# Performance work log

Hardware: AMD Instinct MI355X
Metric: run time of the kernel (lower is better)

Reference implementation:

```python
import jax, jax.numpy as jnp
import numpy as np

B, CH, XL, YL = 512, 1, 64, 64
H = 64                       # num_heads
D = CH * XL * YL             # 4096
F = D // H                   # feature_dim = 64 (== H, required by the mask multiply)


def setup_inputs() -> dict:
    key = jax.random.key(0)
    k1, k2, k3, k4, k5 = jax.random.split(key, 5)
    scale = 1.0 / np.sqrt(D)  # roughly kaiming-ish init for square linears
    return {
        "x": jax.random.normal(k1, (B, CH, XL, YL), dtype=jnp.float32),
        "interface_map": jax.random.uniform(k2, (B, CH, XL, YL), dtype=jnp.float32),
        "Wq": jax.random.normal(k3, (D, D), dtype=jnp.float32) * scale,
        "Wk": jax.random.normal(k4, (D, D), dtype=jnp.float32) * scale,
        "Wv": jax.random.normal(k5, (D, D), dtype=jnp.float32) * scale,
    }


def reference(x, interface_map, Wq, Wk, Wv):
    b = x.shape[0]
    xf = x.reshape(b, D)
    # nn.Linear(bias=False): y = x @ W.T
    q = (xf @ Wq.T).reshape(b, H, F)
    k = (xf @ Wk.T).reshape(b, H, F)
    v = (xf @ Wv.T).reshape(b, H, F)
    inv_sqrt_f = jnp.float32(1.0 / np.sqrt(F))
    qk_t = jnp.einsum("bhf,bgf->bhg", q, k) * inv_sqrt_f           # (B, H, H)
    qk_t = qk_t * interface_map.reshape(b, H, F)                   # multiplicative mask (F == H)
    attention_weights = jax.nn.softmax(qk_t, axis=-1)
    weighted_values = jnp.einsum("bhg,bgf->bhf", attention_weights, v)  # (B, H, F)
    combined = jnp.swapaxes(weighted_values, 1, 2).reshape(b, CH, XL, YL)
    output = x * combined
    return output, attention_weights
```

## Files before the change

### kernel.cpp

```cpp
#include <hip/hip_runtime.h>
#include <cstdint>
#include <cstddef>

typedef __attribute__((ext_vector_type(8))) short short8;
typedef __attribute__((ext_vector_type(4))) float f32x4;

#define NB 512
#define DD 4096

__device__ __forceinline__ unsigned short f2bf(float f) {
    unsigned u = __float_as_uint(f);
    u += 0x7fffu + ((u >> 16) & 1u);
    return (unsigned short)(u >> 16);
}
__device__ __forceinline__ unsigned pack2bf(float a, float b) {
    return (unsigned)f2bf(a) | ((unsigned)f2bf(b) << 16);
}

__device__ __forceinline__ void gload_lds16(const void* g, void* l) {
    __builtin_amdgcn_global_load_lds((const __attribute__((address_space(1))) void*)g,
                                     (__attribute__((address_space(3))) void*)l, 16, 0, 0);
}

__global__ __launch_bounds__(256) void cvt_bf16_kernel(const float* __restrict__ src,
                                                       unsigned short* __restrict__ dst,
                                                       int n8) {
    int i = blockIdx.x * 256 + threadIdx.x;
    if (i >= n8) return;
    const float4* s = (const float4*)src + (size_t)i * 2;
    float4 a = s[0], b = s[1];
    uint4 r;
    r.x = pack2bf(a.x, a.y);
    r.y = pack2bf(a.z, a.w);
    r.z = pack2bf(b.x, b.y);
    r.w = pack2bf(b.z, b.w);
    ((uint4*)dst)[i] = r;
}

__global__ __launch_bounds__(256, 2) void gemm_qkv_kernel(
    const unsigned short* __restrict__ xb,
    const float* __restrict__ w0, const float* __restrict__ w1, const float* __restrict__ w2,
    float* __restrict__ qkv)
{
    const int nt = blockIdx.x;
    const int mt = blockIdx.y;
    const int mz = blockIdx.z;
    const float* W = (mz == 0) ? w0 : ((mz == 1) ? w1 : w2);
    float* C = qkv + (size_t)mz * ((size_t)NB * DD);

    __shared__ unsigned short As[2][128 * 64];
    __shared__ unsigned short Bs[2][128 * 64];

    const int t = threadIdx.x;
    const int l = t & 63;
    const int wv = t >> 6;
    const int wr = wv >> 1, wc = wv & 1;

    const unsigned short* Abase = xb + (size_t)(mt * 128) * DD;
    const float* Wbase = W + (size_t)(nt * 128) * DD;

    f32x4 acc[4][4];
    #pragma unroll
    for (int i = 0; i < 4; ++i)
        #pragma unroll
        for (int j = 0; j < 4; ++j)
            acc[i][j] = (f32x4){0.f, 0.f, 0.f, 0.f};

    float4 breg[8];

    #pragma unroll
    for (int p = 0; p < 8; ++p) {
        int qq = p * 256 + t;
        int row = qq >> 4, c4 = qq & 15;
        breg[p] = *(const float4*)(Wbase + (size_t)row * DD + c4 * 4);
    }
    #pragma unroll
    for (int i = 0; i < 4; ++i) {
        int e = i * 256 + t;
        int r = e >> 3;
        int c = ((e & 7) * 8) ^ ((r & 7) * 8);
        gload_lds16(Abase + (size_t)r * DD + c,
                    (char*)(&As[0][0]) + i * 4096 + wv * 1024);
    }
    #pragma unroll
    for (int p = 0; p < 8; ++p) {
        int qq = p * 256 + t;
        int row = qq >> 4, c4 = qq & 15;
        unsigned short* dst = &Bs[0][row * 64 + ((c4 * 4) ^ ((row & 7) * 8))];
        uint2 pk;
        pk.x = pack2bf(breg[p].x, breg[p].y);
        pk.y = pack2bf(breg[p].z, breg[p].w);
        *(uint2*)dst = pk;
    }
    __syncthreads();

    for (int kt = 0; kt < 64; ++kt) {
        const int cur = kt & 1, nxt = cur ^ 1;
        const int kn = (kt + 1) * 64;
        if (kt < 63) {
            #pragma unroll
            for (int p = 0; p < 8; ++p) {
                int qq = p * 256 + t;
                int row = qq >> 4, c4 = qq & 15;
                breg[p] = *(const float4*)(Wbase + (size_t)row * DD + kn + c4 * 4);
            }
            #pragma unroll
            for (int i = 0; i < 4; ++i) {
                int e = i * 256 + t;
                int r = e >> 3;
                int c = ((e & 7) * 8) ^ ((r & 7) * 8);
                gload_lds16(Abase + (size_t)r * DD + kn + c,
                            (char*)(&As[nxt][0]) + i * 4096 + wv * 1024);
            }
        }
        #pragma unroll
        for (int ks = 0; ks < 2; ++ks) {
            short8 af[4], bf[4];
            #pragma unroll
            for (int fi = 0; fi < 4; ++fi) {
                int row = wr * 64 + fi * 16 + (l & 15);
                int off = row * 64 + ((ks * 32 + (l >> 4) * 8) ^ ((row & 7) * 8));
                af[fi] = *(const short8*)(&As[cur][off]);
            }
            #pragma unroll
            for (int fj = 0; fj < 4; ++fj) {
                int row = wc * 64 + fj * 16 + (l & 15);
                int off = row * 64 + ((ks * 32 + (l >> 4) * 8) ^ ((row & 7) * 8));
                bf[fj] = *(const short8*)(&Bs[cur][off]);
            }
            #pragma unroll
            for (int fi = 0; fi < 4; ++fi)
                #pragma unroll
                for (int fj = 0; fj < 4; ++fj)
                    acc[fi][fj] = __builtin_amdgcn_mfma_f32_16x16x32_bf16(af[fi], bf[fj], acc[fi][fj], 0, 0, 0);
        }
        if (kt < 63) {
            #pragma unroll
            for (int p = 0; p < 8; ++p) {
                int qq = p * 256 + t;
                int row = qq >> 4, c4 = qq & 15;
                unsigned short* dst = &Bs[nxt][row * 64 + ((c4 * 4) ^ ((row & 7) * 8))];
                uint2 pk;
                pk.x = pack2bf(breg[p].x, breg[p].y);
                pk.y = pack2bf(breg[p].z, breg[p].w);
                *(uint2*)dst = pk;
            }
        }
        __syncthreads();
    }

    #pragma unroll
    for (int fi = 0; fi < 4; ++fi) {
        int rbase = mt * 128 + wr * 64 + fi * 16 + (l >> 4) * 4;
        #pragma unroll
        for (int fj = 0; fj < 4; ++fj) {
            int col = nt * 128 + wc * 64 + fj * 16 + (l & 15);
            #pragma unroll
            for (int r = 0; r < 4; ++r)
                C[(size_t)(rbase + r) * DD + col] = acc[fi][fj][r];
        }
    }
}

__global__ __launch_bounds__(256) void attn_kernel(
    const float* __restrict__ qkv,
    const float* __restrict__ x,
    const float* __restrict__ imap,
    float* __restrict__ dout)
{
    const int b = blockIdx.x;
    const int t = threadIdx.x;
    const int l = t & 63;
    const int wv = t >> 6;

    __shared__ float sq[64 * 68];
    __shared__ float sk[64 * 68];
    __shared__ float sv[64 * 68];

    const float* qb = qkv + (size_t)b * DD;
    const float* kb = qkv + (size_t)NB * DD + (size_t)b * DD;
    const float* vb = qkv + 2 * (size_t)NB * DD + (size_t)b * DD;

    #pragma unroll
    for (int i = 0; i < 4; ++i) {
        int f4 = i * 256 + t;
        int r = f4 >> 4, c = (f4 & 15) * 4;
        *(float4*)(&sq[r * 68 + c]) = *(const float4*)(qb + (size_t)f4 * 4);
        *(float4*)(&sk[r * 68 + c]) = *(const float4*)(kb + (size_t)f4 * 4);
        *(float4*)(&sv[r * 68 + c]) = *(const float4*)(vb + (size_t)f4 * 4);
    }
    __syncthreads();

    float accs[16];
    #pragma unroll
    for (int i = 0; i < 16; ++i) accs[i] = 0.f;
    #pragma unroll 4
    for (int f4 = 0; f4 < 16; ++f4) {
        float4 kvv = *(const float4*)(&sk[l * 68 + f4 * 4]);
        #pragma unroll
        for (int i = 0; i < 16; ++i) {
            int h = i * 4 + wv;
            float4 qv = *(const float4*)(&sq[h * 68 + f4 * 4]);
            accs[i] = fmaf(qv.x, kvv.x, fmaf(qv.y, kvv.y, fmaf(qv.z, kvv.z, fmaf(qv.w, kvv.w, accs[i]))));
        }
    }
    __syncthreads();
    #pragma unroll
    for (int i = 0; i < 16; ++i) {
        int h = i * 4 + wv;
        float m = imap[(size_t)b * DD + h * 64 + l];
        sk[h * 65 + l] = accs[i] * 0.125f * m;
    }
    __syncthreads();

    {
        int h = t >> 2, j = t & 3;
        float e[16];
        float mx = -3.0e38f;
        #pragma unroll
        for (int q2 = 0; q2 < 16; ++q2) {
            e[q2] = sk[h * 65 + j * 16 + q2];
            mx = fmaxf(mx, e[q2]);
        }
        mx = fmaxf(mx, __shfl_xor(mx, 1));
        mx = fmaxf(mx, __shfl_xor(mx, 2));
        float s = 0.f;
        #pragma unroll
        for (int q2 = 0; q2 < 16; ++q2) { e[q2] = __expf(e[q2] - mx); s += e[q2]; }
        s += __shfl_xor(s, 1);
        s += __shfl_xor(s, 2);
        float invs = 1.0f / s;
        float* aw = dout + (size_t)NB * DD + (size_t)b * DD + h * 64 + j * 16;
        #pragma unroll
        for (int q2 = 0; q2 < 16; q2 += 4) {
            float4 w4 = {e[q2] * invs, e[q2 + 1] * invs, e[q2 + 2] * invs, e[q2 + 3] * invs};
            *(float4*)(aw + q2) = w4;
            sk[h * 65 + j * 16 + q2 + 0] = w4.x;
            sk[h * 65 + j * 16 + q2 + 1] = w4.y;
            sk[h * 65 + j * 16 + q2 + 2] = w4.z;
            sk[h * 65 + j * 16 + q2 + 3] = w4.w;
        }
    }
    __syncthreads();

    float pacc[16];
    #pragma unroll
    for (int i = 0; i < 16; ++i) pacc[i] = 0.f;
    #pragma unroll 4
    for (int g = 0; g < 64; ++g) {
        float p = sk[l * 65 + g];
        const float4* vr = (const float4*)(&sv[g * 68 + wv * 16]);
        float4 v0 = vr[0], v1 = vr[1], v2 = vr[2], v3 = vr[3];
        pacc[0]  = fmaf(p, v0.x, pacc[0]);
        pacc[1]  = fmaf(p, v0.y, pacc[1]);
        pacc[2]  = fmaf(p, v0.z, pacc[2]);
        pacc[3]  = fmaf(p, v0.w, pacc[3]);
        pacc[4]  = fmaf(p, v1.x, pacc[4]);
        pacc[5]  = fmaf(p, v1.y, pacc[5]);
        pacc[6]  = fmaf(p, v1.z, pacc[6]);
        pacc[7]  = fmaf(p, v1.w, pacc[7]);
        pacc[8]  = fmaf(p, v2.x, pacc[8]);
        pacc[9]  = fmaf(p, v2.y, pacc[9]);
        pacc[10] = fmaf(p, v2.z, pacc[10]);
        pacc[11] = fmaf(p, v2.w, pacc[11]);
        pacc[12] = fmaf(p, v3.x, pacc[12]);
        pacc[13] = fmaf(p, v3.y, pacc[13]);
        pacc[14] = fmaf(p, v3.z, pacc[14]);
        pacc[15] = fmaf(p, v3.w, pacc[15]);
    }
    const size_t ob = (size_t)b * DD + (size_t)(wv * 16) * 64 + l;
    #pragma unroll
    for (int ii = 0; ii < 16; ++ii) {
        size_t o = ob + (size_t)ii * 64;
        dout[o] = x[o] * pacc[ii];
    }
}

extern "C" void kernel_launch(void* const* d_in, const int* in_sizes, int n_in,
                              void* d_out, int out_size, void* d_ws, size_t ws_size,
                              hipStream_t stream) {
    const float* x  = (const float*)d_in[0];
    const float* im = (const float*)d_in[1];
    const float* Wq = (const float*)d_in[2];
    const float* Wk = (const float*)d_in[3];
    const float* Wv = (const float*)d_in[4];
    float* out = (float*)d_out;

    unsigned short* xb = (unsigned short*)d_ws;
    float* qkv = (float*)((char*)d_ws + (size_t)NB * DD * 2);

    cvt_bf16_kernel<<<dim3((NB * DD / 8 + 255) / 256), dim3(256), 0, stream>>>(x, xb, NB * DD / 8);

    dim3 gg(32, 4, 3);
    gemm_qkv_kernel<<<gg, dim3(256), 0, stream>>>(xb, Wq, Wk, Wv, qkv);

    attn_kernel<<<dim3(NB), dim3(256), 0, stream>>>(qkv, x, im, out);
}
```

Baseline: 135.3 us.

## Split-K the QKV GEMM with interleaved output layout and smaller K tiles

The QKV projection GEMM now splits the K dimension in two when the workspace is large enough. That doubles the block count (96x4x2 = 768 blocks) to fill more CUs, and the attention kernel sums the two fp32 partials while loading Q/K/V. The K tile shrinks from 64 to 32, the weight-tile LDS buffer becomes single-buffered, and occupancy is raised to 3 blocks per CU. Q/K/V are stored interleaved per row (stride 12288). The cost is extra partial-sum write and read traffic and an additional barrier per K iteration.

```diff
diff --git a/kernel.cpp b/kernel.cpp
--- a/kernel.cpp
+++ b/kernel.cpp
@@ -7,6 +7,7 @@
 
 #define NB 512
 #define DD 4096
+#define NP 12288
 
 __device__ __forceinline__ unsigned short f2bf(float f) {
     unsigned u = __float_as_uint(f);
@@ -37,28 +38,33 @@
     ((uint4*)dst)[i] = r;
 }
 
-__global__ __launch_bounds__(256, 2) void gemm_qkv_kernel(
+template<int KS>
+__global__ __launch_bounds__(256, 3) void gemm_qkv_kernel(
     const unsigned short* __restrict__ xb,
     const float* __restrict__ w0, const float* __restrict__ w1, const float* __restrict__ w2,
-    float* __restrict__ qkv)
+    float* __restrict__ part)
 {
+    constexpr int KLEN = DD / KS;
+    constexpr int NIT = KLEN / 32;
+
     const int nt = blockIdx.x;
     const int mt = blockIdx.y;
-    const int mz = blockIdx.z;
-    const float* W = (mz == 0) ? w0 : ((mz == 1) ? w1 : w2);
-    float* C = qkv + (size_t)mz * ((size_t)NB * DD);
-
-    __shared__ unsigned short As[2][128 * 64];
-    __shared__ unsigned short Bs[2][128 * 64];
+    const int kz = blockIdx.z;
+
+    const float* W = (nt < 32) ? w0 : ((nt < 64) ? w1 : w2);
+    const int ntl = nt & 31;
+    const float* Wbase = W + (size_t)(ntl * 128) * DD + kz * KLEN;
+    const unsigned short* Abase = xb + (size_t)(mt * 128) * DD + kz * KLEN;
+    float* C = part + (size_t)kz * NB * NP;
+
+    __shared__ unsigned short As[2][128 * 32];
+    __shared__ unsigned short Bs[128 * 32];
 
     const int t = threadIdx.x;
     const int l = t & 63;
     const int wv = t >> 6;
     const int wr = wv >> 1, wc = wv & 1;
 
-    const unsigned short* Abase = xb + (size_t)(mt * 128) * DD;
-    const float* Wbase = W + (size_t)(nt * 128) * DD;
-
     f32x4 acc[4][4];
     #pragma unroll
     for (int i = 0; i < 4; ++i)
@@ -66,85 +72,60 @@
         for (int j = 0; j < 4; ++j)
             acc[i][j] = (f32x4){0.f, 0.f, 0.f, 0.f};
 
-    float4 breg[8];
-
-    #pragma unroll
-    for (int p = 0; p < 8; ++p) {
-        int qq = p * 256 + t;
-        int row = qq >> 4, c4 = qq & 15;
-        breg[p] = *(const float4*)(Wbase + (size_t)row * DD + c4 * 4);
-    }
-    #pragma unroll
-    for (int i = 0; i < 4; ++i) {
-        int e = i * 256 + t;
-        int r = e >> 3;
-        int c = ((e & 7) * 8) ^ ((r & 7) * 8);
-        gload_lds16(Abase + (size_t)r * DD + c,
-                    (char*)(&As[0][0]) + i * 4096 + wv * 1024);
-    }
-    #pragma unroll
-    for (int p = 0; p < 8; ++p) {
-        int qq = p * 256 + t;
-        int row = qq >> 4, c4 = qq & 15;
-        unsigned short* dst = &Bs[0][row * 64 + ((c4 * 4) ^ ((row & 7) * 8))];
-        uint2 pk;
-        pk.x = pack2bf(breg[p].x, breg[p].y);
-        pk.y = pack2bf(breg[p].z, breg[p].w);
-        *(uint2*)dst = pk;
-    }
-    __syncthreads();
-
-    for (int kt = 0; kt < 64; ++kt) {
-        const int cur = kt & 1, nxt = cur ^ 1;
-        const int kn = (kt + 1) * 64;
-        if (kt < 63) {
+    const int arow0 = (t >> 2);
+    const int acol  = (((t & 3) ^ ((t >> 3) & 3)) * 8);
+    const int brow = t >> 1, bh = t & 1;
+    const float* wrow = Wbase + (size_t)brow * DD + bh * 16;
+    const int bws = (t >> 2) & 3;
+    char* bw0 = (char*)(&Bs[0]) + brow * 64 + (((2 * bh) ^ bws) * 16);
+    char* bw1 = (char*)(&Bs[0]) + brow * 64 + (((2 * bh + 1) ^ bws) * 16);
+    const int cx = ((l >> 4) ^ ((l >> 1) & 3));
+
+    float4 breg[4];
+
+    #define LOADB(kt)  { _Pragma("unroll") for (int j = 0; j < 4; ++j) \
+                           breg[j] = *(const float4*)(wrow + (kt) * 32 + j * 4); }
+    #define STAGEA(kt, buf) { _Pragma("unroll") for (int i = 0; i < 2; ++i) \
+                           gload_lds16(Abase + (size_t)(i * 64 + arow0) * DD + (kt) * 32 + acol, \
+                                       (char*)(&As[buf][0]) + i * 4096 + wv * 1024); }
+    #define WRITEB()   { uint4 p0, p1; \
+                         p0.x = pack2bf(breg[0].x, breg[0].y); p0.y = pack2bf(breg[0].z, breg[0].w); \
+                         p0.z = pack2bf(breg[1].x, breg[1].y); p0.w = pack2bf(breg[1].z, breg[1].w); \
+                         p1.x = pack2bf(breg[2].x, breg[2].y); p1.y = pack2bf(breg[2].z, breg[2].w); \
+                         p1.z = pack2bf(breg[3].x, breg[3].y); p1.w = pack2bf(breg[3].z, breg[3].w); \
+                         *(uint4*)bw0 = p0; *(uint4*)bw1 = p1; }
+
+    LOADB(0);
+    STAGEA(0, 0);
+    WRITEB();
+    __syncthreads();
+
+    for (int kt = 0; kt < NIT; ++kt) {
+        const int cur = kt & 1;
+        if (kt + 1 < NIT) {
+            STAGEA(kt + 1, cur ^ 1);
+            LOADB(kt + 1);
+        }
+        short8 af[4], bfr[4];
+        #pragma unroll
+        for (int fi = 0; fi < 4; ++fi) {
+            int row = wr * 64 + fi * 16 + (l & 15);
+            af[fi] = *(const short8*)((const char*)(&As[cur][0]) + row * 64 + cx * 16);
+        }
+        #pragma unroll
+        for (int fj = 0; fj < 4; ++fj) {
+            int row = wc * 64 + fj * 16 + (l & 15);
+            bfr[fj] = *(const short8*)((const char*)(&Bs[0]) + row * 64 + cx * 16);
+        }
+        #pragma unroll
+        for (int fi = 0; fi < 4; ++fi)
             #pragma unroll
-            for (int p = 0; p < 8; ++p) {
-                int qq = p * 256 + t;
-                int row = qq >> 4, c4 = qq & 15;
-                breg[p] = *(const float4*)(Wbase + (size_t)row * DD + kn + c4 * 4);
-            }
-            #pragma unroll
-            for (int i = 0; i < 4; ++i) {
-                int e = i * 256 + t;
-                int r = e >> 3;
-                int c = ((e & 7) * 8) ^ ((r & 7) * 8);
-                gload_lds16(Abase + (size_t)r * DD + kn + c,
-                            (char*)(&As[nxt][0]) + i * 4096 + wv * 1024);
-            }
-        }
-        #pragma unroll
-        for (int ks = 0; ks < 2; ++ks) {
-            short8 af[4], bf[4];
-            #pragma unroll
-            for (int fi = 0; fi < 4; ++fi) {
-                int row = wr * 64 + fi * 16 + (l & 15);
-                int off = row * 64 + ((ks * 32 + (l >> 4) * 8) ^ ((row & 7) * 8));
-                af[fi] = *(const short8*)(&As[cur][off]);
-            }
-            #pragma unroll
-            for (int fj = 0; fj < 4; ++fj) {
-                int row = wc * 64 + fj * 16 + (l & 15);
-                int off = row * 64 + ((ks * 32 + (l >> 4) * 8) ^ ((row & 7) * 8));
-                bf[fj] = *(const short8*)(&Bs[cur][off]);
-            }
-            #pragma unroll
-            for (int fi = 0; fi < 4; ++fi)
-                #pragma unroll
-                for (int fj = 0; fj < 4; ++fj)
-                    acc[fi][fj] = __builtin_amdgcn_mfma_f32_16x16x32_bf16(af[fi], bf[fj], acc[fi][fj], 0, 0, 0);
-        }
-        if (kt < 63) {
-            #pragma unroll
-            for (int p = 0; p < 8; ++p) {
-                int qq = p * 256 + t;
-                int row = qq >> 4, c4 = qq & 15;
-                unsigned short* dst = &Bs[nxt][row * 64 + ((c4 * 4) ^ ((row & 7) * 8))];
-                uint2 pk;
-                pk.x = pack2bf(breg[p].x, breg[p].y);
-                pk.y = pack2bf(breg[p].z, breg[p].w);
-                *(uint2*)dst = pk;
-            }
+            for (int fj = 0; fj < 4; ++fj)
+                acc[fi][fj] = __builtin_amdgcn_mfma_f32_16x16x32_bf16(af[fi], bfr[fj], acc[fi][fj], 0, 0, 0);
+
+        __syncthreads();
+        if (kt + 1 < NIT) {
+            WRITEB();
         }
         __syncthreads();
     }
@@ -157,13 +138,17 @@
             int col = nt * 128 + wc * 64 + fj * 16 + (l & 15);
             #pragma unroll
             for (int r = 0; r < 4; ++r)
-                C[(size_t)(rbase + r) * DD + col] = acc[fi][fj][r];
-        }
-    }
-}
-
+                C[(size_t)(rbase + r) * NP + col] = acc[fi][fj][r];
+        }
+    }
+    #undef LOADB
+    #undef STAGEA
+    #undef WRITEB
+}
+
+template<int KS>
 __global__ __launch_bounds__(256) void attn_kernel(
-    const float* __restrict__ qkv,
+    const float* __restrict__ part,
     const float* __restrict__ x,
     const float* __restrict__ imap,
     float* __restrict__ dout)
@@ -177,17 +162,27 @@
     __shared__ float sk[64 * 68];
     __shared__ float sv[64 * 68];
 
-    const float* qb = qkv + (size_t)b * DD;
-    const float* kb = qkv + (size_t)NB * DD + (size_t)b * DD;
-    const float* vb = qkv + 2 * (size_t)NB * DD + (size_t)b * DD;
+    const float* base0 = part + (size_t)b * NP;
+    const float* base1 = part + (size_t)NB * NP + (size_t)b * NP;
 
     #pragma unroll
     for (int i = 0; i < 4; ++i) {
         int f4 = i * 256 + t;
         int r = f4 >> 4, c = (f4 & 15) * 4;
-        *(float4*)(&sq[r * 68 + c]) = *(const float4*)(qb + (size_t)f4 * 4);
-        *(float4*)(&sk[r * 68 + c]) = *(const float4*)(kb + (size_t)f4 * 4);
-        *(float4*)(&sv[r * 68 + c]) = *(const float4*)(vb + (size_t)f4 * 4);
+        float4 q4 = *(const float4*)(base0 + (size_t)f4 * 4);
+        float4 k4 = *(const float4*)(base0 + DD + (size_t)f4 * 4);
+        float4 v4 = *(const float4*)(base0 + 2 * DD + (size_t)f4 * 4);
+        if (KS == 2) {
+            float4 a4 = *(const float4*)(base1 + (size_t)f4 * 4);
+            float4 b4 = *(const float4*)(base1 + DD + (size_t)f4 * 4);
+            float4 c4 = *(const float4*)(base1 + 2 * DD + (size_t)f4 * 4);
+            q4.x += a4.x; q4.y += a4.y; q4.z += a4.z; q4.w += a4.w;
+            k4.x += b4.x; k4.y += b4.y; k4.z += b4.z; k4.w += b4.w;
+            v4.x += c4.x; v4.y += c4.y; v4.z += c4.z; v4.w += c4.w;
+        }
+        *(float4*)(&sq[r * 68 + c]) = q4;
+        *(float4*)(&sk[r * 68 + c]) = k4;
+        *(float4*)(&sv[r * 68 + c]) = v4;
     }
     __syncthreads();
 
@@ -287,12 +282,18 @@
     float* out = (float*)d_out;
 
     unsigned short* xb = (unsigned short*)d_ws;
-    float* qkv = (float*)((char*)d_ws + (size_t)NB * DD * 2);
+    float* part = (float*)((char*)d_ws + (size_t)NB * DD * 2);
+
+    const size_t need2 = (size_t)NB * DD * 2 + 2ull * NB * NP * 4;
+    const int KS = (ws_size >= need2) ? 2 : 1;
 
     cvt_bf16_kernel<<<dim3((NB * DD / 8 + 255) / 256), dim3(256), 0, stream>>>(x, xb, NB * DD / 8);
 
-    dim3 gg(32, 4, 3);
-    gemm_qkv_kernel<<<gg, dim3(256), 0, stream>>>(xb, Wq, Wk, Wv, qkv);
-
-    attn_kernel<<<dim3(NB), dim3(256), 0, stream>>>(qkv, x, im, out);
-}
+    if (KS == 2) {
+        gemm_qkv_kernel<2><<<dim3(96, 4, 2), dim3(256), 0, stream>>>(xb, Wq, Wk, Wv, part);
+        attn_kernel<2><<<dim3(NB), dim3(256), 0, stream>>>(part, x, im, out);
+    } else {
+        gemm_qkv_kernel<1><<<dim3(96, 4, 1), dim3(256), 0, stream>>>(xb, Wq, Wk, Wv, part);
+        attn_kernel<1><<<dim3(NB), dim3(256), 0, stream>>>(part, x, im, out);
+    }
+}
```

Result: slower. 144.4 us (+6.7%).
